# Performance work log

Hardware: AMD Instinct MI355X
Metric: run time of the kernel (lower is better)

## Reference

```python
import jax, jax.numpy as jnp
import numpy as np

N = 100000     # nodes
E = 1600000    # directed edges
IN, HID, OUT = 128, 64, 64


def setup_inputs() -> dict:
    key = jax.random.key(0)
    k = jax.random.split(key, 6)
    features = jax.random.normal(k[0], (N, IN), dtype=jnp.float32)
    edge_index = jax.random.randint(k[1], (2, E), 0, N, dtype=jnp.int64)
    # Glorot-ish init for linear weights, zeros for bias (PyG GCNConv default)
    W1 = jax.random.normal(k[2], (IN, HID), dtype=jnp.float32) / np.sqrt(IN)
    b1 = jnp.zeros((HID,), dtype=jnp.float32)
    W2 = jax.random.normal(k[3], (HID, OUT), dtype=jnp.float32) / np.sqrt(HID)
    b2 = jnp.zeros((OUT,), dtype=jnp.float32)
    return {"features": features, "edge_index": edge_index, "batch_size": N,
            "W1": W1, "b1": b1, "W2": W2, "b2": b2}


def _gcn_conv(x, W, b, src, dst, n):
    """PyG GCNConv: add self-loops, symmetric deg^-1/2 normalization,
    linear transform then scatter-add aggregation, plus bias."""
    loops = jnp.arange(n, dtype=src.dtype)
    s = jnp.concatenate([src, loops])   # [E+N]
    d = jnp.concatenate([dst, loops])   # [E+N]
    deg = jax.ops.segment_sum(jnp.ones(s.shape, dtype=x.dtype), d, num_segments=n)
    dinv = jnp.where(deg > 0, jax.lax.rsqrt(deg), jnp.zeros_like(deg))
    norm = dinv[s] * dinv[d]            # [E+N]
    h = x @ W                           # [n, out] transform before aggregation
    msg = h[s] * norm[:, None]          # gather + scale  [E+N, out]
    out = jax.ops.segment_sum(msg, d, num_segments=n)  # scatter-add
    return out + b


def reference(features, edge_index, batch_size, W1, b1, W2, b2):
    src, dst = edge_index[0], edge_index[1]
    n = features.shape[0]
    x = _gcn_conv(features, W1, b1, src, dst, n)
    x = jax.nn.relu(x)
    # F.dropout(training=self.training): module is in eval mode -> identity
    x = _gcn_conv(x, W2, b2, src, dst, n)
    return jax.nn.log_softmax(x, axis=1)
```

## Files before the change

kernel.cpp:

```cpp
#include <hip/hip_runtime.h>
#include <math.h>

#define K1 128
#define C  64
#define SCAN_B 1024

__global__ void detect_kernel(const int* __restrict__ e, int twoE, int* __restrict__ flag) {
    __shared__ int nz;
    if (threadIdx.x == 0) nz = 0;
    __syncthreads();
    int nchk = twoE / 2; if (nchk > 4096) nchk = 4096;
    int bad = 0;
    for (int i = threadIdx.x; i < nchk; i += blockDim.x)
        if (e[2 * i + 1] != 0) bad = 1;
    if (bad) atomicOr(&nz, 1);
    __syncthreads();
    if (threadIdx.x == 0) *flag = nz ? 0 : 1;
}

__global__ void convert_kernel(const void* __restrict__ ein, int twoE,
                               const int* __restrict__ flag, int* __restrict__ eout) {
    int is64 = *flag;
    int i = blockIdx.x * blockDim.x + threadIdx.x;
    int stride = gridDim.x * blockDim.x;
    if (is64) {
        const long long* p = (const long long*)ein;
        for (; i < twoE; i += stride) eout[i] = (int)p[i];
    } else {
        const int* p = (const int*)ein;
        for (; i < twoE; i += stride) eout[i] = p[i];
    }
}

__global__ void zero_kernel(int* __restrict__ p, int n) {
    for (int i = blockIdx.x * blockDim.x + threadIdx.x; i < n; i += gridDim.x * blockDim.x)
        p[i] = 0;
}

__global__ void cnt_kernel(const int* __restrict__ dst, int E, int* __restrict__ cnt) {
    for (int e = blockIdx.x * blockDim.x + threadIdx.x; e < E; e += gridDim.x * blockDim.x)
        atomicAdd(&cnt[dst[e]], 1);
}

__global__ void dinv_kernel(const int* __restrict__ cnt, float* __restrict__ dinv, int n) {
    for (int i = blockIdx.x * blockDim.x + threadIdx.x; i < n; i += gridDim.x * blockDim.x)
        dinv[i] = rsqrtf((float)(cnt[i] + 1));
}

__global__ __launch_bounds__(SCAN_B) void scan1_kernel(const int* __restrict__ cnt, int n,
        int* __restrict__ ex, int* __restrict__ bsum) {
    __shared__ int s[SCAN_B];
    int i = blockIdx.x * SCAN_B + threadIdx.x;
    int v = (i < n) ? cnt[i] : 0;
    s[threadIdx.x] = v;
    __syncthreads();
    for (int off = 1; off < SCAN_B; off <<= 1) {
        int t = (threadIdx.x >= off) ? s[threadIdx.x - off] : 0;
        __syncthreads();
        s[threadIdx.x] += t;
        __syncthreads();
    }
    if (i < n) ex[i] = s[threadIdx.x] - v;
    if (threadIdx.x == SCAN_B - 1) bsum[blockIdx.x] = s[SCAN_B - 1];
}

__global__ void scan2_kernel(int* __restrict__ bsum, int nb) {
    const int lane = threadIdx.x & 63;
    int acc = 0;
    for (int base = 0; base < nb; base += 64) {
        int v = (base + lane < nb) ? bsum[base + lane] : 0;
        int sc = v;
        #pragma unroll
        for (int off = 1; off < 64; off <<= 1) {
            int t = __shfl_up(sc, off, 64);
            if (lane >= off) sc += t;
        }
        if (base + lane < nb) bsum[base + lane] = acc + sc - v;
        acc += __shfl(sc, 63, 64);
    }
}

__global__ void scan3_kernel(int* __restrict__ ex, const int* __restrict__ bsum,
                             int* __restrict__ fill, int n, int Etot) {
    for (int i = blockIdx.x * blockDim.x + threadIdx.x; i < n; i += gridDim.x * blockDim.x) {
        int v = ex[i] + bsum[i / SCAN_B];
        ex[i] = v;
        fill[i] = v;
    }
    if (blockIdx.x == 0 && threadIdx.x == 0) ex[n] = Etot;
}

__global__ void scatter_kernel(const int* __restrict__ src, const int* __restrict__ dst,
                               int E, int* __restrict__ fill, int* __restrict__ csr) {
    for (int e = blockIdx.x * blockDim.x + threadIdx.x; e < E; e += gridDim.x * blockDim.x) {
        int pos = atomicAdd(&fill[dst[e]], 1);
        csr[pos] = src[e];
    }
}

template<int K, int R>
__global__ __launch_bounds__(256) void gemm_kernel(const float* __restrict__ X,
        const float* __restrict__ W, const float* __restrict__ dinv,
        float* __restrict__ G, int n)
{
    __shared__ float Ws[K * C];
    for (int i = threadIdx.x; i < K * C; i += 256) Ws[i] = W[i];
    __syncthreads();
    const int lane = threadIdx.x & 63;
    const int wave = __builtin_amdgcn_readfirstlane((int)(threadIdx.x >> 6));
    const int waves = gridDim.x * 4;
    for (int base = (blockIdx.x * 4 + wave) * R; base < n; base += waves * R) {
        float acc[R];
        #pragma unroll
        for (int r = 0; r < R; ++r) acc[r] = 0.0f;
        if (base + R <= n) {
            for (int k = 0; k < K; ++k) {
                float w = Ws[k * C + lane];
                #pragma unroll
                for (int r = 0; r < R; ++r)
                    acc[r] = fmaf(X[(size_t)(base + r) * K + k], w, acc[r]);
            }
            #pragma unroll
            for (int r = 0; r < R; ++r)
                G[(size_t)(base + r) * C + lane] = acc[r] * dinv[base + r];
        } else {
            for (int r = 0; r < R; ++r) {
                if (base + r >= n) break;
                float a = 0.0f;
                for (int k = 0; k < K; ++k)
                    a = fmaf(X[(size_t)(base + r) * K + k], Ws[k * C + lane], a);
                G[(size_t)(base + r) * C + lane] = a * dinv[base + r];
            }
        }
    }
}

template<int MODE>
__global__ __launch_bounds__(256) void gather_kernel(const int* __restrict__ rowptr,
        const int* __restrict__ csr, const float* __restrict__ G,
        const float* __restrict__ dinv, const float* __restrict__ bias,
        float* __restrict__ Out, int n)
{
    const int lane = threadIdx.x & 63;
    const int v = __builtin_amdgcn_readfirstlane((int)(blockIdx.x * 4 + (threadIdx.x >> 6)));
    if (v >= n) return;
    const int start = __builtin_amdgcn_readfirstlane(rowptr[v]);
    const int end   = __builtin_amdgcn_readfirstlane(rowptr[v + 1]);
    float a0 = G[(size_t)v * C + lane];
    float a1 = 0.f, a2 = 0.f, a3 = 0.f;
    for (int base = start; base < end; base += 64) {
        int m = end - base; if (m > 64) m = 64;
        int idx = (lane < m) ? csr[base + lane] : 0;
        int j = 0;
        for (; j + 4 <= m; j += 4) {
            int s0 = __shfl(idx, j,     64);
            int s1 = __shfl(idx, j + 1, 64);
            int s2 = __shfl(idx, j + 2, 64);
            int s3 = __shfl(idx, j + 3, 64);
            a0 += G[(size_t)s0 * C + lane];
            a1 += G[(size_t)s1 * C + lane];
            a2 += G[(size_t)s2 * C + lane];
            a3 += G[(size_t)s3 * C + lane];
        }
        for (; j < m; ++j) {
            int s = __shfl(idx, j, 64);
            a0 += G[(size_t)s * C + lane];
        }
    }
    float acc = (a0 + a1) + (a2 + a3);
    float y = fmaf(acc, dinv[v], bias[lane]);
    if (MODE == 0) {
        Out[(size_t)v * C + lane] = y > 0.f ? y : 0.f;
    } else {
        float mx = y;
        #pragma unroll
        for (int off = 32; off > 0; off >>= 1) mx = fmaxf(mx, __shfl_xor(mx, off, 64));
        float ex = expf(y - mx);
        float l = ex;
        #pragma unroll
        for (int off = 32; off > 0; off >>= 1) l += __shfl_xor(l, off, 64);
        Out[(size_t)v * C + lane] = y - mx - logf(l);
    }
}

static inline size_t align16(size_t x) { return (x + 15) & ~(size_t)15; }

extern "C" void kernel_launch(void* const* d_in, const int* in_sizes, int n_in,
                              void* d_out, int out_size, void* d_ws, size_t ws_size,
                              hipStream_t stream)
{
    const float* X  = (const float*)d_in[0];
    const void*  EI = d_in[1];
    const float* W1 = (const float*)d_in[3];
    const float* b1 = (const float*)d_in[4];
    const float* W2 = (const float*)d_in[5];
    const float* b2 = (const float*)d_in[6];
    float* Out = (float*)d_out;

    const int n    = in_sizes[0] / K1;
    const int E    = in_sizes[1] / 2;
    const int twoE = 2 * E;
    const int nb   = (n + SCAN_B - 1) / SCAN_B;

    char* ws = (char*)d_ws;
    size_t off = 0;
    int*   edges  = (int*)(ws + off); off = align16(off + (size_t)twoE * 4);
    int*   csr    = (int*)(ws + off); off = align16(off + (size_t)E * 4);
    int*   rowptr = (int*)(ws + off); off = align16(off + (size_t)(n + 1) * 4);
    int*   cnt    = (int*)(ws + off); off = align16(off + (size_t)n * 4);
    int*   bsum   = (int*)(ws + off); off = align16(off + (size_t)(nb + 1) * 4);
    int*   flag   = (int*)(ws + off); off = align16(off + 16);
    float* dinv   = (float*)(ws + off); off = align16(off + (size_t)n * 4);
    float* G      = (float*)(ws + off); off = align16(off + (size_t)n * C * 4);
    int*   fill   = cnt;
    float* H      = Out;

    const int* srcp = edges;
    const int* dstp = edges + E;

    hipLaunchKernelGGL(detect_kernel,  dim3(1),    dim3(256), 0, stream, (const int*)EI, twoE, flag);
    hipLaunchKernelGGL(convert_kernel, dim3(4096), dim3(256), 0, stream, EI, twoE, flag, edges);

    hipLaunchKernelGGL(zero_kernel, dim3(512),  dim3(256), 0, stream, cnt, n);
    hipLaunchKernelGGL(cnt_kernel,  dim3(2048), dim3(256), 0, stream, dstp, E, cnt);
    hipLaunchKernelGGL(dinv_kernel, dim3(512),  dim3(256), 0, stream, cnt, dinv, n);
    hipLaunchKernelGGL(scan1_kernel, dim3(nb), dim3(SCAN_B), 0, stream, cnt, n, rowptr, bsum);
    hipLaunchKernelGGL(scan2_kernel, dim3(1),  dim3(64),     0, stream, bsum, nb);
    hipLaunchKernelGGL(scan3_kernel, dim3(1024), dim3(256),  0, stream, rowptr, bsum, fill, n, E);
    hipLaunchKernelGGL(scatter_kernel, dim3(2048), dim3(256), 0, stream, srcp, dstp, E, fill, csr);

    const int ngb = (n + 3) / 4;

    hipLaunchKernelGGL((gemm_kernel<K1, 8>), dim3(2048), dim3(256), 0, stream, X, W1, dinv, G, n);
    hipLaunchKernelGGL((gather_kernel<0>), dim3(ngb), dim3(256), 0, stream, rowptr, csr, G, dinv, b1, H, n);

    hipLaunchKernelGGL((gemm_kernel<C, 8>), dim3(2048), dim3(256), 0, stream, H, W2, dinv, G, n);
    hipLaunchKernelGGL((gather_kernel<1>), dim3(ngb), dim3(256), 0, stream, rowptr, csr, G, dinv, b2, Out, n);
}
```

Measured before the change: 583.4 us.

## Build CSR via two-level bucketed scatter and store transformed features in fp16

```diff
diff --git a/kernel.cpp b/kernel.cpp
--- a/kernel.cpp
+++ b/kernel.cpp
@@ -1,9 +1,15 @@
 #include <hip/hip_runtime.h>
+#include <hip/hip_fp16.h>
 #include <math.h>
 
 #define K1 128
 #define C  64
 #define SCAN_B 1024
+#define NBMAX  256
+#define BSH    9
+#define WIDTH  512
+#define DEPTH  28
+#define FLUSH_TILES 8
 
 __global__ void detect_kernel(const int* __restrict__ e, int twoE, int* __restrict__ flag) {
     __shared__ int nz;
@@ -18,37 +24,33 @@
     if (threadIdx.x == 0) *flag = nz ? 0 : 1;
 }
 
-__global__ void convert_kernel(const void* __restrict__ ein, int twoE,
-                               const int* __restrict__ flag, int* __restrict__ eout) {
-    int is64 = *flag;
-    int i = blockIdx.x * blockDim.x + threadIdx.x;
-    int stride = gridDim.x * blockDim.x;
-    if (is64) {
-        const long long* p = (const long long*)ein;
-        for (; i < twoE; i += stride) eout[i] = (int)p[i];
-    } else {
-        const int* p = (const int*)ein;
-        for (; i < twoE; i += stride) eout[i] = p[i];
-    }
-}
-
-__global__ void zero_kernel(int* __restrict__ p, int n) {
-    for (int i = blockIdx.x * blockDim.x + threadIdx.x; i < n; i += gridDim.x * blockDim.x)
-        p[i] = 0;
-}
-
-__global__ void cnt_kernel(const int* __restrict__ dst, int E, int* __restrict__ cnt) {
-    for (int e = blockIdx.x * blockDim.x + threadIdx.x; e < E; e += gridDim.x * blockDim.x)
-        atomicAdd(&cnt[dst[e]], 1);
-}
-
-__global__ void dinv_kernel(const int* __restrict__ cnt, float* __restrict__ dinv, int n) {
-    for (int i = blockIdx.x * blockDim.x + threadIdx.x; i < n; i += gridDim.x * blockDim.x)
-        dinv[i] = rsqrtf((float)(cnt[i] + 1));
+__device__ __forceinline__ int load_dst(const void* EI, int E, int e, int is64) {
+    return is64 ? (int)((const long long*)EI)[(size_t)E + e] : ((const int*)EI)[(size_t)E + e];
+}
+__device__ __forceinline__ int load_src(const void* EI, int E, int e, int is64) {
+    return is64 ? (int)((const long long*)EI)[e] : ((const int*)EI)[e];
+}
+
+__global__ __launch_bounds__(256) void hist_kernel(const void* __restrict__ EI, int E,
+        const int* __restrict__ flag, int* __restrict__ cnt, int* __restrict__ bcnt,
+        int nbuckets) {
+    __shared__ int bh[NBMAX];
+    for (int i = threadIdx.x; i < NBMAX; i += 256) bh[i] = 0;
+    __syncthreads();
+    const int is64 = *flag;
+    for (int e = blockIdx.x * 256 + threadIdx.x; e < E; e += gridDim.x * 256) {
+        int d = load_dst(EI, E, e, is64);
+        atomicAdd(&cnt[d], 1);
+        int b = d >> BSH;
+        if (b < NBMAX) atomicAdd(&bh[b], 1);
+    }
+    __syncthreads();
+    for (int i = threadIdx.x; i < nbuckets; i += 256)
+        if (bh[i]) atomicAdd(&bcnt[i], bh[i]);
 }
 
 __global__ __launch_bounds__(SCAN_B) void scan1_kernel(const int* __restrict__ cnt, int n,
-        int* __restrict__ ex, int* __restrict__ bsum) {
+        int* __restrict__ ex, int* __restrict__ bsum, float* __restrict__ dinv) {
     __shared__ int s[SCAN_B];
     int i = blockIdx.x * SCAN_B + threadIdx.x;
     int v = (i < n) ? cnt[i] : 0;
@@ -60,48 +62,133 @@
         s[threadIdx.x] += t;
         __syncthreads();
     }
-    if (i < n) ex[i] = s[threadIdx.x] - v;
+    if (i < n) {
+        ex[i] = s[threadIdx.x] - v;
+        dinv[i] = rsqrtf((float)(v + 1));
+    }
     if (threadIdx.x == SCAN_B - 1) bsum[blockIdx.x] = s[SCAN_B - 1];
 }
 
-__global__ void scan2_kernel(int* __restrict__ bsum, int nb) {
+__global__ void scan2_kernel(int* __restrict__ bsum, int nb,
+        const int* __restrict__ bcnt, int* __restrict__ bbase, int* __restrict__ tail,
+        int nbuckets, int Etot) {
     const int lane = threadIdx.x & 63;
-    int acc = 0;
-    for (int base = 0; base < nb; base += 64) {
-        int v = (base + lane < nb) ? bsum[base + lane] : 0;
-        int sc = v;
-        #pragma unroll
-        for (int off = 1; off < 64; off <<= 1) {
-            int t = __shfl_up(sc, off, 64);
-            if (lane >= off) sc += t;
-        }
-        if (base + lane < nb) bsum[base + lane] = acc + sc - v;
-        acc += __shfl(sc, 63, 64);
+    const int wv = threadIdx.x >> 6;
+    if (wv == 0) {
+        int acc = 0;
+        for (int base = 0; base < nb; base += 64) {
+            int v = (base + lane < nb) ? bsum[base + lane] : 0;
+            int sc = v;
+            #pragma unroll
+            for (int off = 1; off < 64; off <<= 1) {
+                int t = __shfl_up(sc, off, 64);
+                if (lane >= off) sc += t;
+            }
+            if (base + lane < nb) bsum[base + lane] = acc + sc - v;
+            acc += __shfl(sc, 63, 64);
+        }
+    } else if (wv == 1) {
+        int acc = 0;
+        for (int base = 0; base < nbuckets; base += 64) {
+            int v = (base + lane < nbuckets) ? bcnt[base + lane] : 0;
+            int sc = v;
+            #pragma unroll
+            for (int off = 1; off < 64; off <<= 1) {
+                int t = __shfl_up(sc, off, 64);
+                if (lane >= off) sc += t;
+            }
+            if (base + lane < nbuckets) {
+                int ex = acc + sc - v;
+                bbase[base + lane] = ex;
+                tail[base + lane] = ex;
+            }
+            acc += __shfl(sc, 63, 64);
+        }
+        if (lane == 0) bbase[nbuckets] = Etot;
     }
 }
 
 __global__ void scan3_kernel(int* __restrict__ ex, const int* __restrict__ bsum,
-                             int* __restrict__ fill, int n, int Etot) {
-    for (int i = blockIdx.x * blockDim.x + threadIdx.x; i < n; i += gridDim.x * blockDim.x) {
-        int v = ex[i] + bsum[i / SCAN_B];
-        ex[i] = v;
-        fill[i] = v;
-    }
+                             int n, int Etot) {
+    for (int i = blockIdx.x * blockDim.x + threadIdx.x; i < n; i += gridDim.x * blockDim.x)
+        ex[i] += bsum[i / SCAN_B];
     if (blockIdx.x == 0 && threadIdx.x == 0) ex[n] = Etot;
 }
 
-__global__ void scatter_kernel(const int* __restrict__ src, const int* __restrict__ dst,
-                               int E, int* __restrict__ fill, int* __restrict__ csr) {
-    for (int e = blockIdx.x * blockDim.x + threadIdx.x; e < E; e += gridDim.x * blockDim.x) {
-        int pos = atomicAdd(&fill[dst[e]], 1);
-        csr[pos] = src[e];
+__global__ __launch_bounds__(256) void bucket_kernel(const void* __restrict__ EI, int E,
+        const int* __restrict__ flag, uint2* __restrict__ pairs, int* __restrict__ tail,
+        int nbuckets) {
+    __shared__ uint2 stage[NBMAX][DEPTH];
+    __shared__ int scnt[NBMAX];
+    for (int i = threadIdx.x; i < NBMAX; i += 256) scnt[i] = 0;
+    __syncthreads();
+    const int is64 = *flag;
+    const int tid = threadIdx.x;
+    const int lane = tid & 63;
+    const int wv = tid >> 6;
+    int chunk = (E + gridDim.x - 1) / gridDim.x;
+    int start = blockIdx.x * chunk;
+    int end = start + chunk; if (end > E) end = E;
+
+#define FLUSH_STAGE()                                                         \
+    do {                                                                      \
+        __syncthreads();                                                      \
+        for (int b = wv; b < nbuckets; b += 4) {                              \
+            int c = scnt[b]; if (c > DEPTH) c = DEPTH;                        \
+            if (c > 0) {                                                      \
+                int bse = 0;                                                  \
+                if (lane == 0) bse = atomicAdd(&tail[b], c);                  \
+                bse = __shfl(bse, 0, 64);                                     \
+                if (lane < c) pairs[bse + lane] = stage[b][lane];             \
+            }                                                                 \
+        }                                                                     \
+        __syncthreads();                                                      \
+        for (int i = tid; i < NBMAX; i += 256) scnt[i] = 0;                   \
+        __syncthreads();                                                      \
+    } while (0)
+
+    int tilecnt = 0;
+    for (int base = start; base < end; base += 256) {
+        int e = base + tid;
+        if (e < end) {
+            int d = load_dst(EI, E, e, is64);
+            int s = load_src(EI, E, e, is64);
+            int b = d >> BSH;
+            int slot = (b < NBMAX) ? atomicAdd(&scnt[b], 1) : DEPTH;
+            if (slot < DEPTH) {
+                stage[b][slot] = make_uint2((unsigned)d, (unsigned)s);
+            } else {
+                int pos = atomicAdd(&tail[b], 1);
+                pairs[pos] = make_uint2((unsigned)d, (unsigned)s);
+            }
+        }
+        if (++tilecnt == FLUSH_TILES) { tilecnt = 0; FLUSH_STAGE(); }
+    }
+    FLUSH_STAGE();
+#undef FLUSH_STAGE
+}
+
+__global__ __launch_bounds__(256) void scatterlocal_kernel(const uint2* __restrict__ pairs,
+        const int* __restrict__ bbase, const int* __restrict__ rowptr,
+        int* __restrict__ csr, int n) {
+    __shared__ int fillL[WIDTH];
+    const int b = blockIdx.x;
+    const int nb0 = b << BSH;
+    int nodes = n - nb0; if (nodes > WIDTH) nodes = WIDTH;
+    for (int i = threadIdx.x; i < nodes; i += 256) fillL[i] = rowptr[nb0 + i];
+    __syncthreads();
+    const int s0 = bbase[b], s1 = bbase[b + 1];
+    for (int i = s0 + threadIdx.x; i < s1; i += 256) {
+        uint2 p = pairs[i];
+        int pos = atomicAdd(&fillL[(int)p.x - nb0], 1);
+        csr[pos] = (int)p.y;
     }
 }
 
 template<int K, int R>
 __global__ __launch_bounds__(256) void gemm_kernel(const float* __restrict__ X,
         const float* __restrict__ W, const float* __restrict__ dinv,
-        float* __restrict__ G, int n)
+        __half* __restrict__ G, int n)
 {
     __shared__ float Ws[K * C];
     for (int i = threadIdx.x; i < K * C; i += 256) Ws[i] = W[i];
@@ -122,14 +209,14 @@
             }
             #pragma unroll
             for (int r = 0; r < R; ++r)
-                G[(size_t)(base + r) * C + lane] = acc[r] * dinv[base + r];
+                G[(size_t)(base + r) * C + lane] = __float2half_rn(acc[r] * dinv[base + r]);
         } else {
             for (int r = 0; r < R; ++r) {
                 if (base + r >= n) break;
                 float a = 0.0f;
                 for (int k = 0; k < K; ++k)
                     a = fmaf(X[(size_t)(base + r) * K + k], Ws[k * C + lane], a);
-                G[(size_t)(base + r) * C + lane] = a * dinv[base + r];
+                G[(size_t)(base + r) * C + lane] = __float2half_rn(a * dinv[base + r]);
             }
         }
     }
@@ -137,7 +224,7 @@
 
 template<int MODE>
 __global__ __launch_bounds__(256) void gather_kernel(const int* __restrict__ rowptr,
-        const int* __restrict__ csr, const float* __restrict__ G,
+        const int* __restrict__ csr, const __half* __restrict__ G,
         const float* __restrict__ dinv, const float* __restrict__ bias,
         float* __restrict__ Out, int n)
 {
@@ -146,7 +233,7 @@
     if (v >= n) return;
     const int start = __builtin_amdgcn_readfirstlane(rowptr[v]);
     const int end   = __builtin_amdgcn_readfirstlane(rowptr[v + 1]);
-    float a0 = G[(size_t)v * C + lane];
+    float a0 = __half2float(G[(size_t)v * C + lane]);
     float a1 = 0.f, a2 = 0.f, a3 = 0.f;
     for (int base = start; base < end; base += 64) {
         int m = end - base; if (m > 64) m = 64;
@@ -157,14 +244,14 @@
             int s1 = __shfl(idx, j + 1, 64);
             int s2 = __shfl(idx, j + 2, 64);
             int s3 = __shfl(idx, j + 3, 64);
-            a0 += G[(size_t)s0 * C + lane];
-            a1 += G[(size_t)s1 * C + lane];
-            a2 += G[(size_t)s2 * C + lane];
-            a3 += G[(size_t)s3 * C + lane];
+            a0 += __half2float(G[(size_t)s0 * C + lane]);
+            a1 += __half2float(G[(size_t)s1 * C + lane]);
+            a2 += __half2float(G[(size_t)s2 * C + lane]);
+            a3 += __half2float(G[(size_t)s3 * C + lane]);
         }
         for (; j < m; ++j) {
             int s = __shfl(idx, j, 64);
-            a0 += G[(size_t)s * C + lane];
+            a0 += __half2float(G[(size_t)s * C + lane]);
         }
     }
     float acc = (a0 + a1) + (a2 + a3);
@@ -201,33 +288,32 @@
     const int E    = in_sizes[1] / 2;
     const int twoE = 2 * E;
     const int nb   = (n + SCAN_B - 1) / SCAN_B;
+    const int nbuckets = (n + WIDTH - 1) >> BSH;
 
     char* ws = (char*)d_ws;
     size_t off = 0;
-    int*   edges  = (int*)(ws + off); off = align16(off + (size_t)twoE * 4);
-    int*   csr    = (int*)(ws + off); off = align16(off + (size_t)E * 4);
-    int*   rowptr = (int*)(ws + off); off = align16(off + (size_t)(n + 1) * 4);
-    int*   cnt    = (int*)(ws + off); off = align16(off + (size_t)n * 4);
-    int*   bsum   = (int*)(ws + off); off = align16(off + (size_t)(nb + 1) * 4);
-    int*   flag   = (int*)(ws + off); off = align16(off + 16);
+    uint2* pairs  = (uint2*)(ws + off); off = align16(off + (size_t)E * 8);
+    int*   csr    = (int*)(ws + off);   off = align16(off + (size_t)E * 4);
+    int*   rowptr = (int*)(ws + off);   off = align16(off + (size_t)(n + 1) * 4);
+    int*   cnt    = (int*)(ws + off);   off += (size_t)n * 4;
+    int*   bcnt   = (int*)(ws + off);   off = align16(off + (size_t)NBMAX * 4);
+    int*   bsum   = (int*)(ws + off);   off = align16(off + (size_t)(nb + 1) * 4);
+    int*   bbase  = (int*)(ws + off);   off = align16(off + (size_t)(NBMAX + 1) * 4);
+    int*   tail   = (int*)(ws + off);   off = align16(off + (size_t)NBMAX * 4);
+    int*   flag   = (int*)(ws + off);   off = align16(off + 16);
     float* dinv   = (float*)(ws + off); off = align16(off + (size_t)n * 4);
-    float* G      = (float*)(ws + off); off = align16(off + (size_t)n * C * 4);
-    int*   fill   = cnt;
+    __half* G     = (__half*)(ws + off); off = align16(off + (size_t)n * C * 2);
     float* H      = Out;
 
-    const int* srcp = edges;
-    const int* dstp = edges + E;
-
-    hipLaunchKernelGGL(detect_kernel,  dim3(1),    dim3(256), 0, stream, (const int*)EI, twoE, flag);
-    hipLaunchKernelGGL(convert_kernel, dim3(4096), dim3(256), 0, stream, EI, twoE, flag, edges);
-
-    hipLaunchKernelGGL(zero_kernel, dim3(512),  dim3(256), 0, stream, cnt, n);
-    hipLaunchKernelGGL(cnt_kernel,  dim3(2048), dim3(256), 0, stream, dstp, E, cnt);
-    hipLaunchKernelGGL(dinv_kernel, dim3(512),  dim3(256), 0, stream, cnt, dinv, n);
-    hipLaunchKernelGGL(scan1_kernel, dim3(nb), dim3(SCAN_B), 0, stream, cnt, n, rowptr, bsum);
-    hipLaunchKernelGGL(scan2_kernel, dim3(1),  dim3(64),     0, stream, bsum, nb);
-    hipLaunchKernelGGL(scan3_kernel, dim3(1024), dim3(256),  0, stream, rowptr, bsum, fill, n, E);
-    hipLaunchKernelGGL(scatter_kernel, dim3(2048), dim3(256), 0, stream, srcp, dstp, E, fill, csr);
+    hipLaunchKernelGGL(detect_kernel, dim3(1), dim3(256), 0, stream, (const int*)EI, twoE, flag);
+    hipMemsetAsync(cnt, 0, ((size_t)n + NBMAX) * 4, stream);
+
+    hipLaunchKernelGGL(hist_kernel,  dim3(1024), dim3(256), 0, stream, EI, E, flag, cnt, bcnt, nbuckets);
+    hipLaunchKernelGGL(scan1_kernel, dim3(nb), dim3(SCAN_B), 0, stream, cnt, n, rowptr, bsum, dinv);
+    hipLaunchKernelGGL(scan2_kernel, dim3(1), dim3(128), 0, stream, bsum, nb, bcnt, bbase, tail, nbuckets, E);
+    hipLaunchKernelGGL(scan3_kernel, dim3(1024), dim3(256), 0, stream, rowptr, bsum, n, E);
+    hipLaunchKernelGGL(bucket_kernel, dim3(512), dim3(256), 0, stream, EI, E, flag, pairs, tail, nbuckets);
+    hipLaunchKernelGGL(scatterlocal_kernel, dim3(nbuckets), dim3(256), 0, stream, pairs, bbase, rowptr, csr, n);
 
     const int ngb = (n + 3) / 4;
 
```

New measurement: 1.136 ms. +94.7%, slower.
